# Kernel optimization log

Measured on AMD Instinct MI355X. Metric: run time of the kernel, lower is better.

The kernel has to match this reference:

```python
import jax, jax.numpy as jnp
import numpy as np

N = 50000          # nodes
E = 800000         # edges (before self-loops)
F_IN = 128         # num_features
HID = 16           # hidden_dim (per head)
HEADS = 4
NG = 128           # number of graphs in batch
NC = 10            # num_classes
LAYERS = 3
NEG_SLOPE = 0.2    # PyG GATConv default
EPS = 1e-16


def setup_inputs() -> dict:
    key = jax.random.key(0)
    ks = jax.random.split(key, 4 + 4 * LAYERS + 2)
    inp = {}
    inp["x"] = jax.random.normal(ks[0], (N, F_IN), jnp.float32)
    inp["edge_index"] = jax.random.randint(ks[1], (2, E), 0, N, dtype=jnp.int32)
    inp["batch"] = jnp.sort(jax.random.randint(ks[2], (N,), 0, NG, dtype=jnp.int32))
    in_dims = [F_IN] + [HID * HEADS] * (LAYERS - 1)
    for i in range(LAYERS):
        kb = 3 + 4 * i
        s = 1.0 / np.sqrt(in_dims[i])
        inp[f"W{i}"] = jax.random.normal(ks[kb], (in_dims[i], HEADS * HID), jnp.float32) * s
        inp[f"b{i}"] = jnp.zeros((HEADS * HID,), jnp.float32)
        inp[f"as{i}"] = jax.random.normal(ks[kb + 1], (HEADS, HID), jnp.float32) * 0.1
        inp[f"ad{i}"] = jax.random.normal(ks[kb + 2], (HEADS, HID), jnp.float32) * 0.1
    inp["Wr"] = jax.random.normal(ks[3 + 4 * LAYERS], (HEADS * HID, NC), jnp.float32) * (1.0 / np.sqrt(HEADS * HID))
    inp["br"] = jnp.zeros((NC,), jnp.float32)
    return inp


def _gat_layer(x, src, dst, W, b, att_src, att_dst):
    n = x.shape[0]
    h = (x @ W).reshape(n, HEADS, HID)                # [N,H,D]
    a_src = jnp.einsum('nhd,hd->nh', h, att_src)      # [N,H]
    a_dst = jnp.einsum('nhd,hd->nh', h, att_dst)
    logits = jax.nn.leaky_relu(a_src[src] + a_dst[dst], NEG_SLOPE)  # [E,H]
    # segment softmax over destination node
    m = jax.ops.segment_max(logits, dst, num_segments=n)
    e = jnp.exp(logits - m[dst])
    s = jax.ops.segment_sum(e, dst, num_segments=n)
    alpha = e / (s[dst] + EPS)                        # [E,H]
    msg = h[src] * alpha[:, :, None]                  # [E,H,D]
    out = jax.ops.segment_sum(msg, dst, num_segments=n)
    return out.reshape(n, HEADS * HID) + b


def reference(x, edge_index, batch,
              W0, b0, as0, ad0,
              W1, b1, as1, ad1,
              W2, b2, as2, ad2,
              Wr, br):
    # add self loops (PyG GATConv default add_self_loops=True)
    loop = jnp.arange(N, dtype=edge_index.dtype)
    src = jnp.concatenate([edge_index[0], loop])
    dst = jnp.concatenate([edge_index[1], loop])
    params = [(W0, b0, as0, ad0), (W1, b1, as1, ad1), (W2, b2, as2, ad2)]
    h = x
    for (W, b, a_s, a_d) in params:
        h = _gat_layer(h, src, dst, W, b, a_s, a_d)
        h = jax.nn.silu(h)
        # dropout p=0.0 (eval): identity
    pooled = jax.ops.segment_sum(h, batch, num_segments=NG)   # [NG, H*D]
    logits = jax.nn.relu(pooled @ Wr + br)                    # make_mlp ends with ReLU
    return jax.nn.log_softmax(logits, axis=1)
```

## Files before the change

### kernel.cpp

```cpp
#include <hip/hip_runtime.h>
#include <hip/hip_fp16.h>
#include <cstdint>
#include <cstddef>

#define HEADS 4
#define HID 16
#define HD 64
#define NCLS 10
#define NGRAPH 128
#define NEG_SLOPE 0.2f
#define SM_EPS 1e-16f
#define SLOTS 128
#define SCAT_BLOCKS 2048

static inline size_t alignup(size_t x) { return (x + 255) & ~size_t(255); }

__device__ __forceinline__ unsigned short f2h(float f) {
    __half h = __float2half(f);
    return *reinterpret_cast<unsigned short*>(&h);
}

__global__ __launch_bounds__(256) void fused0_kernel(
        const float* __restrict__ in, const float* __restrict__ Wp,
        const float* __restrict__ as_, const float* __restrict__ ad_,
        unsigned short* __restrict__ hb, float* __restrict__ asrc,
        float* __restrict__ adst, int N, int K, int ntiles,
        const int* __restrict__ srcA, const int* __restrict__ dstA,
        int E, int npg, int* __restrict__ cursor,
        unsigned short* __restrict__ csr_src) {
    __shared__ __align__(16) float xs[64][68];
    __shared__ __align__(16) float Ws[64][64];
    __shared__ float avl[HD], adl[HD];

    if ((int)blockIdx.x >= ntiles) {
        int bid = blockIdx.x - ntiles;
        int g = bid & 7;
        int c = bid >> 3;
        int nchunks = SCAT_BLOCKS >> 3;
        int chunk = (E + nchunks - 1) / nchunks;
        int start = c * chunk;
        int end = min(E, start + chunk);
        int lo = g * npg, hi = lo + npg;
        for (int e = start + threadIdx.x; e < end; e += blockDim.x) {
            int d = dstA[e];
            if (d >= lo && d < hi) {
                int pos = atomicAdd(&cursor[d], 1);
                if (pos < SLOTS) csr_src[(size_t)d * SLOTS + pos] = (unsigned short)srcA[e];
            }
        }
        return;
    }

    int tid = threadIdx.x, lane = tid & 63, wave = tid >> 6;
    int cg = lane & 15;
    int c0 = cg * 4;
    int r0 = wave * 16 + (lane >> 4) * 4;
    if (tid < HD) { avl[tid] = as_[tid]; adl[tid] = ad_[tid]; }

    int base = blockIdx.x * 64;
    float acc[4][4];
#pragma unroll
    for (int i = 0; i < 4; i++)
#pragma unroll
        for (int j = 0; j < 4; j++) acc[i][j] = 0.f;

    for (int kh = 0; kh < K; kh += 64) {
        __syncthreads();
        for (int i = tid; i < 1024; i += 256) {
            int r = i >> 4, c = (i & 15) * 4;
            float4 v = make_float4(0.f, 0.f, 0.f, 0.f);
            if (base + r < N) v = *(const float4*)(in + (size_t)(base + r) * K + kh + c);
            *(float4*)&xs[r][c] = v;
        }
        for (int i = tid; i < 1024; i += 256) {
            int r = i >> 4, c = (i & 15) * 4;
            *(float4*)&Ws[r][c] = *(const float4*)(Wp + (size_t)(kh + r) * HD + c);
        }
        __syncthreads();

#pragma unroll 8
        for (int k = 0; k < 64; k += 4) {
            float4 wv[4], xv[4];
#pragma unroll
            for (int j = 0; j < 4; j++) wv[j] = *(const float4*)&Ws[k + j][c0];
#pragma unroll
            for (int i = 0; i < 4; i++) xv[i] = *(const float4*)&xs[r0 + i][k];
#pragma unroll
            for (int i = 0; i < 4; i++) {
                acc[i][0] += xv[i].x * wv[0].x + xv[i].y * wv[1].x + xv[i].z * wv[2].x + xv[i].w * wv[3].x;
                acc[i][1] += xv[i].x * wv[0].y + xv[i].y * wv[1].y + xv[i].z * wv[2].y + xv[i].w * wv[3].y;
                acc[i][2] += xv[i].x * wv[0].z + xv[i].y * wv[1].z + xv[i].z * wv[2].z + xv[i].w * wv[3].z;
                acc[i][3] += xv[i].x * wv[0].w + xv[i].y * wv[1].w + xv[i].z * wv[2].w + xv[i].w * wv[3].w;
            }
        }
    }

    int head = cg >> 2;
#pragma unroll
    for (int i = 0; i < 4; i++) {
        int node = base + r0 + i;
        float s = acc[i][0] * avl[c0] + acc[i][1] * avl[c0 + 1] +
                  acc[i][2] * avl[c0 + 2] + acc[i][3] * avl[c0 + 3];
        float d = acc[i][0] * adl[c0] + acc[i][1] * adl[c0 + 1] +
                  acc[i][2] * adl[c0 + 2] + acc[i][3] * adl[c0 + 3];
        s += __shfl_xor(s, 1); s += __shfl_xor(s, 2);
        d += __shfl_xor(d, 1); d += __shfl_xor(d, 2);
        if (node < N) {
            ushort4 pk;
            pk.x = f2h(acc[i][0]); pk.y = f2h(acc[i][1]);
            pk.z = f2h(acc[i][2]); pk.w = f2h(acc[i][3]);
            *(ushort4*)&hb[(size_t)node * HD + c0] = pk;
            if ((cg & 3) == 0) {
                asrc[node * HEADS + head] = s;
                adst[node * HEADS + head] = d;
            }
        }
    }
}

__global__ __launch_bounds__(256) void gemm_attn_kernel(
        const float* __restrict__ in, const float* __restrict__ Wp,
        const float* __restrict__ as_, const float* __restrict__ ad_,
        unsigned short* __restrict__ hb, float* __restrict__ asrc,
        float* __restrict__ adst, int N, int K) {
    __shared__ __align__(16) float xs[64][68];
    __shared__ __align__(16) float Ws[64][64];
    __shared__ float avl[HD], adl[HD];
    int tid = threadIdx.x, lane = tid & 63, wave = tid >> 6;
    int cg = lane & 15;
    int c0 = cg * 4;
    int r0 = wave * 16 + (lane >> 4) * 4;
    if (tid < HD) { avl[tid] = as_[tid]; adl[tid] = ad_[tid]; }

    int base = blockIdx.x * 64;
    float acc[4][4];
#pragma unroll
    for (int i = 0; i < 4; i++)
#pragma unroll
        for (int j = 0; j < 4; j++) acc[i][j] = 0.f;

    for (int kh = 0; kh < K; kh += 64) {
        __syncthreads();
        for (int i = tid; i < 1024; i += 256) {
            int r = i >> 4, c = (i & 15) * 4;
            float4 v = make_float4(0.f, 0.f, 0.f, 0.f);
            if (base + r < N) v = *(const float4*)(in + (size_t)(base + r) * K + kh + c);
            *(float4*)&xs[r][c] = v;
        }
        for (int i = tid; i < 1024; i += 256) {
            int r = i >> 4, c = (i & 15) * 4;
            *(float4*)&Ws[r][c] = *(const float4*)(Wp + (size_t)(kh + r) * HD + c);
        }
        __syncthreads();

#pragma unroll 8
        for (int k = 0; k < 64; k += 4) {
            float4 wv[4], xv[4];
#pragma unroll
            for (int j = 0; j < 4; j++) wv[j] = *(const float4*)&Ws[k + j][c0];
#pragma unroll
            for (int i = 0; i < 4; i++) xv[i] = *(const float4*)&xs[r0 + i][k];
#pragma unroll
            for (int i = 0; i < 4; i++) {
                acc[i][0] += xv[i].x * wv[0].x + xv[i].y * wv[1].x + xv[i].z * wv[2].x + xv[i].w * wv[3].x;
                acc[i][1] += xv[i].x * wv[0].y + xv[i].y * wv[1].y + xv[i].z * wv[2].y + xv[i].w * wv[3].y;
                acc[i][2] += xv[i].x * wv[0].z + xv[i].y * wv[1].z + xv[i].z * wv[2].z + xv[i].w * wv[3].z;
                acc[i][3] += xv[i].x * wv[0].w + xv[i].y * wv[1].w + xv[i].z * wv[2].w + xv[i].w * wv[3].w;
            }
        }
    }

    int head = cg >> 2;
#pragma unroll
    for (int i = 0; i < 4; i++) {
        int node = base + r0 + i;
        float s = acc[i][0] * avl[c0] + acc[i][1] * avl[c0 + 1] +
                  acc[i][2] * avl[c0 + 2] + acc[i][3] * avl[c0 + 3];
        float d = acc[i][0] * adl[c0] + acc[i][1] * adl[c0 + 1] +
                  acc[i][2] * adl[c0 + 2] + acc[i][3] * adl[c0 + 3];
        s += __shfl_xor(s, 1); s += __shfl_xor(s, 2);
        d += __shfl_xor(d, 1); d += __shfl_xor(d, 2);
        if (node < N) {
            ushort4 pk;
            pk.x = f2h(acc[i][0]); pk.y = f2h(acc[i][1]);
            pk.z = f2h(acc[i][2]); pk.w = f2h(acc[i][3]);
            *(ushort4*)&hb[(size_t)node * HD + c0] = pk;
            if ((cg & 3) == 0) {
                asrc[node * HEADS + head] = s;
                adst[node * HEADS + head] = d;
            }
        }
    }
}

__global__ void gat_gather_kernel(const int* __restrict__ deg,
                                  const unsigned short* __restrict__ csr_src,
                                  int N, const unsigned short* __restrict__ hb,
                                  const float* __restrict__ asrc, const float* __restrict__ adst,
                                  const float* __restrict__ bias, float* __restrict__ out) {
    long long gw = (blockIdx.x * (long long)blockDim.x + threadIdx.x) >> 6;
    int wid0 = (int)(gw << 1);
    if (wid0 >= N) return;
    int wid1 = wid0 + 1;
    bool has1 = wid1 < N;
    int wb1 = has1 ? wid1 : wid0;
    int lane = threadIdx.x & 63;
    int hh = lane & 3;
    int eg = lane >> 2;
    int e2 = lane >> 5;
    int cp = lane & 31;
    int headc = cp >> 3;

    int cnt0 = min(deg[wid0], SLOTS);
    int cnt1 = has1 ? min(deg[wid1], SLOTS) : 0;

    float4 as0 = *(const float4*)&asrc[wid0 * 4];
    float4 ad0 = *(const float4*)&adst[wid0 * 4];
    float p00 = as0.x + ad0.x; p00 = p00 > 0.f ? p00 : NEG_SLOPE * p00;
    float p01 = as0.y + ad0.y; p01 = p01 > 0.f ? p01 : NEG_SLOPE * p01;
    float p02 = as0.z + ad0.z; p02 = p02 > 0.f ? p02 : NEG_SLOPE * p02;
    float p03 = as0.w + ad0.w; p03 = p03 > 0.f ? p03 : NEG_SLOPE * p03;
    float lS0 = (hh == 0) ? p00 : (hh == 1) ? p01 : (hh == 2) ? p02 : p03;
    float adh0 = (hh == 0) ? ad0.x : (hh == 1) ? ad0.y : (hh == 2) ? ad0.z : ad0.w;

    float4 as1 = *(const float4*)&asrc[wb1 * 4];
    float4 ad1 = *(const float4*)&adst[wb1 * 4];
    float p10 = as1.x + ad1.x; p10 = p10 > 0.f ? p10 : NEG_SLOPE * p10;
    float p11 = as1.y + ad1.y; p11 = p11 > 0.f ? p11 : NEG_SLOPE * p11;
    float p12 = as1.z + ad1.z; p12 = p12 > 0.f ? p12 : NEG_SLOPE * p12;
    float p13 = as1.w + ad1.w; p13 = p13 > 0.f ? p13 : NEG_SLOPE * p13;
    float lS1 = (hh == 0) ? p10 : (hh == 1) ? p11 : (hh == 2) ? p12 : p13;
    float adh1 = (hh == 0) ? ad1.x : (hh == 1) ? ad1.y : (hh == 2) ? ad1.z : ad1.w;

    float dsum0 = 0.f, dsum1 = 0.f;
    float2 a0 = make_float2(0.f, 0.f), a1 = make_float2(0.f, 0.f);

    if (e2 == 0) {
        __half2 hw = *(const __half2*)&hb[(unsigned)(wid0 * HD + 2 * cp)];
        a0.x = __half2float(hw.x);
        a0.y = __half2float(hw.y);
    } else {
        __half2 hw = *(const __half2*)&hb[(unsigned)(wb1 * HD + 2 * cp)];
        a1.x = __half2float(hw.x);
        a1.y = __half2float(hw.y);
    }

    int nch = max((cnt0 + 15) >> 4, (cnt1 + 15) >> 4);
    for (int ch = 0; ch < nch; ch++) {
        int idx = (ch << 4) + eg;
        unsigned pk0 = (unsigned)wid0 << 16;
        unsigned pk1 = (unsigned)wb1 << 16;
        float w0 = 0.f, w1 = 0.f;
        if (idx < cnt0) {
            int s = (int)csr_src[(size_t)wid0 * SLOTS + idx];
            float l = asrc[(unsigned)(s * HEADS + hh)] + adh0;
            l = (l > 0.f) ? l : NEG_SLOPE * l;
            w0 = __expf(l - lS0);
            pk0 = ((unsigned)s << 16) | ((__float_as_uint(w0) + 0x8000u) >> 16);
        }
        if (idx < cnt1) {
            int s = (int)csr_src[(size_t)wid1 * SLOTS + idx];
            float l = asrc[(unsigned)(s * HEADS + hh)] + adh1;
            l = (l > 0.f) ? l : NEG_SLOPE * l;
            w1 = __expf(l - lS1);
            pk1 = ((unsigned)s << 16) | ((__float_as_uint(w1) + 0x8000u) >> 16);
        }
        dsum0 += w0;
        dsum1 += w1;

        unsigned pp0[8], pp1[8];
        __half2 hw0[8], hw1[8];
#pragma unroll
        for (int j = 0; j < 8; j++) pp0[j] = (unsigned)__shfl((int)pk0, (e2 * 8 + j) * 4 + headc);
#pragma unroll
        for (int j = 0; j < 8; j++) pp1[j] = (unsigned)__shfl((int)pk1, (e2 * 8 + j) * 4 + headc);
#pragma unroll
        for (int j = 0; j < 8; j++) hw0[j] = *(const __half2*)&hb[(pp0[j] >> 16) * HD + 2 * cp];
#pragma unroll
        for (int j = 0; j < 8; j++) hw1[j] = *(const __half2*)&hb[(pp1[j] >> 16) * HD + 2 * cp];
#pragma unroll
        for (int j = 0; j < 8; j++) {
            float wj0 = __uint_as_float(pp0[j] << 16);
            float wj1 = __uint_as_float(pp1[j] << 16);
            a0.x += wj0 * __half2float(hw0[j].x);
            a0.y += wj0 * __half2float(hw0[j].y);
            a1.x += wj1 * __half2float(hw1[j].x);
            a1.y += wj1 * __half2float(hw1[j].y);
        }
    }

    a0.x += __shfl_xor(a0.x, 32);
    a0.y += __shfl_xor(a0.y, 32);
    a1.x += __shfl_xor(a1.x, 32);
    a1.y += __shfl_xor(a1.y, 32);

    dsum0 += __shfl_xor(dsum0, 4);
    dsum0 += __shfl_xor(dsum0, 8);
    dsum0 += __shfl_xor(dsum0, 16);
    dsum0 += __shfl_xor(dsum0, 32);
    dsum1 += __shfl_xor(dsum1, 4);
    dsum1 += __shfl_xor(dsum1, 8);
    dsum1 += __shfl_xor(dsum1, 16);
    dsum1 += __shfl_xor(dsum1, 32);
    float ssum0 = __shfl(dsum0, headc) + 1.0f;
    float ssum1 = __shfl(dsum1, headc) + 1.0f;

    float2 bb2 = *(const float2*)&bias[2 * cp];
    if (e2 == 0) {
        float vx = a0.x / (ssum0 + SM_EPS) + bb2.x;
        float vy = a0.y / (ssum0 + SM_EPS) + bb2.y;
        float2 o;
        o.x = vx / (1.f + expf(-vx));
        o.y = vy / (1.f + expf(-vy));
        *(float2*)&out[(size_t)wid0 * HD + 2 * cp] = o;
    } else if (has1) {
        float vx = a1.x / (ssum1 + SM_EPS) + bb2.x;
        float vy = a1.y / (ssum1 + SM_EPS) + bb2.y;
        float2 o;
        o.x = vx / (1.f + expf(-vx));
        o.y = vy / (1.f + expf(-vy));
        *(float2*)&out[(size_t)wid1 * HD + 2 * cp] = o;
    }
}

__global__ void pool_kernel(const float* __restrict__ h, const int* __restrict__ batch,
                            float* __restrict__ pooled, int N) {
    int gw = (int)((blockIdx.x * (long long)blockDim.x + threadIdx.x) >> 6);
    int lane = threadIdx.x & 63;
    int n_begin = gw * 64;
    if (n_begin >= N) return;
    int n_end = min(n_begin + 64, N);
    float acc = 0.f;
    int g = batch[n_begin];
    for (int n = n_begin; n < n_end; n++) {
        int gn = batch[n];
        if (gn != g) {
            atomicAdd(&pooled[(size_t)g * HD + lane], acc);
            acc = 0.f;
            g = gn;
        }
        acc += h[(size_t)n * HD + lane];
    }
    atomicAdd(&pooled[(size_t)g * HD + lane], acc);
}

__global__ void head_kernel(const float* __restrict__ pooled, const float* __restrict__ Wr,
                            const float* __restrict__ br, float* __restrict__ out) {
    int g = threadIdx.x;
    if (g >= NGRAPH) return;
    float l[NCLS];
    float mx = -1e30f;
#pragma unroll
    for (int c = 0; c < NCLS; c++) {
        float a = br[c];
        for (int k = 0; k < HD; k++) a += pooled[(size_t)g * HD + k] * Wr[k * NCLS + c];
        a = (a > 0.f) ? a : 0.f;
        l[c] = a;
        mx = fmaxf(mx, a);
    }
    float se = 0.f;
#pragma unroll
    for (int c = 0; c < NCLS; c++) se += expf(l[c] - mx);
    float lse = logf(se);
#pragma unroll
    for (int c = 0; c < NCLS; c++) out[(size_t)g * NCLS + c] = l[c] - mx - lse;
}

extern "C" void kernel_launch(void* const* d_in, const int* in_sizes, int n_in,
                              void* d_out, int out_size, void* d_ws, size_t ws_size,
                              hipStream_t stream) {
    const float* x = (const float*)d_in[0];
    const int* ei = (const int*)d_in[1];
    const int* batch = (const int*)d_in[2];
    const float* W[3]  = {(const float*)d_in[3], (const float*)d_in[7],  (const float*)d_in[11]};
    const float* bb[3] = {(const float*)d_in[4], (const float*)d_in[8],  (const float*)d_in[12]};
    const float* as_[3] = {(const float*)d_in[5], (const float*)d_in[9], (const float*)d_in[13]};
    const float* ad_[3] = {(const float*)d_in[6], (const float*)d_in[10], (const float*)d_in[14]};
    const float* Wr = (const float*)d_in[15];
    const float* br = (const float*)d_in[16];

    const int N = in_sizes[2];
    const int E = in_sizes[1] / 2;
    const int F0 = in_sizes[0] / N;

    char* p = (char*)d_ws;
    unsigned short* hb = (unsigned short*)p; p += alignup((size_t)N * HD * 2);
    float* hbuf  = (float*)p; p += alignup((size_t)N * HD * 4);
    float* asrc  = (float*)p; p += alignup((size_t)N * HEADS * 4);
    float* adst  = (float*)p; p += alignup((size_t)N * HEADS * 4);
    int* cursor  = (int*)p;   p += alignup((size_t)N * 4);
    unsigned short* csr_src = (unsigned short*)p; p += alignup((size_t)N * SLOTS * 2);
    float* pooled = (float*)p; p += alignup((size_t)NGRAPH * HD * 4);

    const int* srcA = ei;
    const int* dstA = ei + E;

    int ntiles = (N + 63) / 64;
    int npg = (N + 7) / 8;
    int gather_blocks = (int)((((long long)(N + 1) / 2) * 64 + 255) / 256);

    hipMemsetAsync(cursor, 0, (size_t)N * 4, stream);
    fused0_kernel<<<ntiles + SCAT_BLOCKS, 256, 0, stream>>>(
        x, W[0], as_[0], ad_[0], hb, asrc, adst, N, F0, ntiles,
        srcA, dstA, E, npg, cursor, csr_src);
    gat_gather_kernel<<<gather_blocks, 256, 0, stream>>>(cursor, csr_src, N, hb,
                                                         asrc, adst, bb[0], hbuf);

    for (int layer = 1; layer < 3; layer++) {
        gemm_attn_kernel<<<ntiles, 256, 0, stream>>>(hbuf, W[layer], as_[layer], ad_[layer],
                                                     hb, asrc, adst, N, HD);
        gat_gather_kernel<<<gather_blocks, 256, 0, stream>>>(cursor, csr_src, N, hb,
                                                             asrc, adst, bb[layer], hbuf);
    }

    hipMemsetAsync(pooled, 0, (size_t)NGRAPH * HD * 4, stream);
    int pool_waves = (N + 63) / 64;
    pool_kernel<<<(pool_waves * 64 + 255) / 256, 256, 0, stream>>>(hbuf, batch, pooled, N);
    head_kernel<<<1, 128, 0, stream>>>(pooled, Wr, br, (float*)d_out);
}
```

Before: 239.7 us.

## Split fused layer-0 GEMM and edge scatter back into separate kernels

Removes the horizontally fused kernel that ran the layer-0 GEMM tiles and the CSR edge-scatter blocks in one launch. The scatter now runs as its own kernel before the layer loop, and layer 0 reuses the generic gemm_attn_kernel. This drops the fused kernel's branch and frees the scatter blocks from the GEMM kernel's launch bounds and shared-memory allocation, at the cost of one extra launch and no overlap between GEMM and scatter work.

```diff
diff --git a/kernel.cpp b/kernel.cpp
--- a/kernel.cpp
+++ b/kernel.cpp
@@ -11,7 +11,6 @@
 #define NEG_SLOPE 0.2f
 #define SM_EPS 1e-16f
 #define SLOTS 128
-#define SCAT_BLOCKS 2048
 
 static inline size_t alignup(size_t x) { return (x + 255) & ~size_t(255); }
 
@@ -20,37 +19,34 @@
     return *reinterpret_cast<unsigned short*>(&h);
 }
 
-__global__ __launch_bounds__(256) void fused0_kernel(
+__global__ void scatter_kernel(const int* __restrict__ srcA, const int* __restrict__ dstA,
+                               int E, int npg, int* __restrict__ cursor,
+                               unsigned short* __restrict__ csr_src) {
+    int g = blockIdx.x & 7;
+    int c = blockIdx.x >> 3;
+    int nchunks = gridDim.x >> 3;
+    int chunk = (E + nchunks - 1) / nchunks;
+    int start = c * chunk;
+    int end = min(E, start + chunk);
+    int lo = g * npg, hi = lo + npg;
+    for (int e = start + threadIdx.x; e < end; e += blockDim.x) {
+        int d = dstA[e];
+        if (d >= lo && d < hi) {
+            int pos = atomicAdd(&cursor[d], 1);
+            if (pos < SLOTS) csr_src[(size_t)d * SLOTS + pos] = (unsigned short)srcA[e];
+        }
+    }
+}
+
+
+__global__ __launch_bounds__(256) void gemm_attn_kernel(
         const float* __restrict__ in, const float* __restrict__ Wp,
         const float* __restrict__ as_, const float* __restrict__ ad_,
         unsigned short* __restrict__ hb, float* __restrict__ asrc,
-        float* __restrict__ adst, int N, int K, int ntiles,
-        const int* __restrict__ srcA, const int* __restrict__ dstA,
-        int E, int npg, int* __restrict__ cursor,
-        unsigned short* __restrict__ csr_src) {
+        float* __restrict__ adst, int N, int K) {
     __shared__ __align__(16) float xs[64][68];
     __shared__ __align__(16) float Ws[64][64];
     __shared__ float avl[HD], adl[HD];
-
-    if ((int)blockIdx.x >= ntiles) {
-        int bid = blockIdx.x - ntiles;
-        int g = bid & 7;
-        int c = bid >> 3;
-        int nchunks = SCAT_BLOCKS >> 3;
-        int chunk = (E + nchunks - 1) / nchunks;
-        int start = c * chunk;
-        int end = min(E, start + chunk);
-        int lo = g * npg, hi = lo + npg;
-        for (int e = start + threadIdx.x; e < end; e += blockDim.x) {
-            int d = dstA[e];
-            if (d >= lo && d < hi) {
-                int pos = atomicAdd(&cursor[d], 1);
-                if (pos < SLOTS) csr_src[(size_t)d * SLOTS + pos] = (unsigned short)srcA[e];
-            }
-        }
-        return;
-    }
-
     int tid = threadIdx.x, lane = tid & 63, wave = tid >> 6;
     int cg = lane & 15;
     int c0 = cg * 4;
@@ -118,81 +114,6 @@
     }
 }
 
-__global__ __launch_bounds__(256) void gemm_attn_kernel(
-        const float* __restrict__ in, const float* __restrict__ Wp,
-        const float* __restrict__ as_, const float* __restrict__ ad_,
-        unsigned short* __restrict__ hb, float* __restrict__ asrc,
-        float* __restrict__ adst, int N, int K) {
-    __shared__ __align__(16) float xs[64][68];
-    __shared__ __align__(16) float Ws[64][64];
-    __shared__ float avl[HD], adl[HD];
-    int tid = threadIdx.x, lane = tid & 63, wave = tid >> 6;
-    int cg = lane & 15;
-    int c0 = cg * 4;
-    int r0 = wave * 16 + (lane >> 4) * 4;
-    if (tid < HD) { avl[tid] = as_[tid]; adl[tid] = ad_[tid]; }
-
-    int base = blockIdx.x * 64;
-    float acc[4][4];
-#pragma unroll
-    for (int i = 0; i < 4; i++)
-#pragma unroll
-        for (int j = 0; j < 4; j++) acc[i][j] = 0.f;
-
-    for (int kh = 0; kh < K; kh += 64) {
-        __syncthreads();
-        for (int i = tid; i < 1024; i += 256) {
-            int r = i >> 4, c = (i & 15) * 4;
-            float4 v = make_float4(0.f, 0.f, 0.f, 0.f);
-            if (base + r < N) v = *(const float4*)(in + (size_t)(base + r) * K + kh + c);
-            *(float4*)&xs[r][c] = v;
-        }
-        for (int i = tid; i < 1024; i += 256) {
-            int r = i >> 4, c = (i & 15) * 4;
-            *(float4*)&Ws[r][c] = *(const float4*)(Wp + (size_t)(kh + r) * HD + c);
-        }
-        __syncthreads();
-
-#pragma unroll 8
-        for (int k = 0; k < 64; k += 4) {
-            float4 wv[4], xv[4];
-#pragma unroll
-            for (int j = 0; j < 4; j++) wv[j] = *(const float4*)&Ws[k + j][c0];
-#pragma unroll
-            for (int i = 0; i < 4; i++) xv[i] = *(const float4*)&xs[r0 + i][k];
-#pragma unroll
-            for (int i = 0; i < 4; i++) {
-                acc[i][0] += xv[i].x * wv[0].x + xv[i].y * wv[1].x + xv[i].z * wv[2].x + xv[i].w * wv[3].x;
-                acc[i][1] += xv[i].x * wv[0].y + xv[i].y * wv[1].y + xv[i].z * wv[2].y + xv[i].w * wv[3].y;
-                acc[i][2] += xv[i].x * wv[0].z + xv[i].y * wv[1].z + xv[i].z * wv[2].z + xv[i].w * wv[3].z;
-                acc[i][3] += xv[i].x * wv[0].w + xv[i].y * wv[1].w + xv[i].z * wv[2].w + xv[i].w * wv[3].w;
-            }
-        }
-    }
-
-    int head = cg >> 2;
-#pragma unroll
-    for (int i = 0; i < 4; i++) {
-        int node = base + r0 + i;
-        float s = acc[i][0] * avl[c0] + acc[i][1] * avl[c0 + 1] +
-                  acc[i][2] * avl[c0 + 2] + acc[i][3] * avl[c0 + 3];
-        float d = acc[i][0] * adl[c0] + acc[i][1] * adl[c0 + 1] +
-                  acc[i][2] * adl[c0 + 2] + acc[i][3] * adl[c0 + 3];
-        s += __shfl_xor(s, 1); s += __shfl_xor(s, 2);
-        d += __shfl_xor(d, 1); d += __shfl_xor(d, 2);
-        if (node < N) {
-            ushort4 pk;
-            pk.x = f2h(acc[i][0]); pk.y = f2h(acc[i][1]);
-            pk.z = f2h(acc[i][2]); pk.w = f2h(acc[i][3]);
-            *(ushort4*)&hb[(size_t)node * HD + c0] = pk;
-            if ((cg & 3) == 0) {
-                asrc[node * HEADS + head] = s;
-                adst[node * HEADS + head] = d;
-            }
-        }
-    }
-}
-
 __global__ void gat_gather_kernel(const int* __restrict__ deg,
                                   const unsigned short* __restrict__ csr_src,
                                   int N, const unsigned short* __restrict__ hb,
@@ -400,15 +321,13 @@
     int gather_blocks = (int)((((long long)(N + 1) / 2) * 64 + 255) / 256);
 
     hipMemsetAsync(cursor, 0, (size_t)N * 4, stream);
-    fused0_kernel<<<ntiles + SCAT_BLOCKS, 256, 0, stream>>>(
-        x, W[0], as_[0], ad_[0], hb, asrc, adst, N, F0, ntiles,
-        srcA, dstA, E, npg, cursor, csr_src);
-    gat_gather_kernel<<<gather_blocks, 256, 0, stream>>>(cursor, csr_src, N, hb,
-                                                         asrc, adst, bb[0], hbuf);
-
-    for (int layer = 1; layer < 3; layer++) {
-        gemm_attn_kernel<<<ntiles, 256, 0, stream>>>(hbuf, W[layer], as_[layer], ad_[layer],
-                                                     hb, asrc, adst, N, HD);
+    scatter_kernel<<<2048, 256, 0, stream>>>(srcA, dstA, E, npg, cursor, csr_src);
+
+    for (int layer = 0; layer < 3; layer++) {
+        const float* in = (layer == 0) ? x : hbuf;
+        int K = (layer == 0) ? F0 : HD;
+        gemm_attn_kernel<<<ntiles, 256, 0, stream>>>(in, W[layer], as_[layer], ad_[layer],
+                                                     hb, asrc, adst, N, K);
         gat_gather_kernel<<<gather_blocks, 256, 0, stream>>>(cursor, csr_src, N, hb,
                                                              asrc, adst, bb[layer], hbuf);
     }
```

Measured after the change: 247.6 us. +3.3%, slower.
